# Kernel optimization log

Hardware: AMD Instinct MI355X
Metric: run time of the kernel (lower is better)

The kernel has to match this reference:

```python
import jax, jax.numpy as jnp
import numpy as np

TEAM = 5
N_PLAYER = 131072
PD = 256
HD = 256
MLP_H = 512
B = 16384

def _combine(t=TEAM):
    i1, i2 = [], []
    for i in range(t):
        for j in range(t):
            if i != j:
                i1.append(i); i2.append(j)
    return np.array(i1), np.array(i2)

IDX1, IDX2 = _combine()

def setup_inputs() -> dict:
    key = jax.random.key(0)
    ks = jax.random.split(key, 12)
    def xavier(k, shape):
        fan_in, fan_out = shape[1], shape[0]
        std = np.sqrt(2.0 / (fan_in + fan_out))
        return (jax.random.normal(k, shape, dtype=jnp.float32) * std)
    return {
        'team_ids': jax.random.randint(ks[0], (B, TEAM), 0, N_PLAYER),
        'emb': xavier(ks[1], (N_PLAYER, PD)),
        'fm_w1': xavier(ks[2], (2 * HD, PD)),
        'fm_b1': jnp.zeros((2 * HD,), jnp.float32),
        'fm_w2': xavier(ks[3], (HD, 2 * HD)),
        'fm_b2': jnp.zeros((HD,), jnp.float32),
        'att_w': xavier(ks[4], (HD, HD)),
        'att_b': jnp.zeros((HD,), jnp.float32),
        'mlp_w1': xavier(ks[5], (MLP_H, HD)),
        'mlp_b1': jnp.zeros((MLP_H,), jnp.float32),
        'mlp_w2': xavier(ks[6], (1, MLP_H)),
        'mlp_b2': jnp.zeros((1,), jnp.float32),
    }

def reference(team_ids, emb, fm_w1, fm_b1, fm_w2, fm_b2, att_w, att_b,
              mlp_w1, mlp_b1, mlp_w2, mlp_b2):
    # embedding lookup: [B, 5, PD]
    x = emb[team_ids]
    # feature mapper: Linear -> SiLU -> Linear  => [B, 5, HD]
    h = jax.nn.silu(jnp.einsum('btp,hp->bth', x, fm_w1) + fm_b1)
    h = jnp.einsum('bth,oh->bto', h, fm_w2) + fm_b2
    # pairwise gather (20 ordered pairs): [B, 20, HD]
    a = h[:, IDX1]
    b = h[:, IDX2]
    prod = a * b
    # small MLP (dropout is inference identity): [B, 20]
    m = jax.nn.silu(jnp.einsum('bph,mh->bpm', prod, mlp_w1) + mlp_b1)
    order2 = (jnp.einsum('bpm,om->bpo', m, mlp_w2) + mlp_b2)[..., 0]
    # attention (reduce=True -> view [B, 5, 4, HD], softmax over axis 2)
    wa = jnp.einsum('bph,oh->bpo', a, att_w) + att_b
    score = (wa * b).sum(-1).reshape(-1, TEAM, TEAM - 1)
    normal = jax.nn.softmax(score, axis=2).reshape(-1, TEAM * (TEAM - 1))
    order2 = order2 * normal
    return order2.sum(axis=1, keepdims=True)  # [B, 1]
```

## Files before the change

kernel.cpp:

```cpp
#include <hip/hip_runtime.h>

#define NB     16384
#define TEAM   5
#define NPAIR  20
#define UPAIR  10
#define PD     256
#define HD     256
#define H1D    512
#define NPLAY  (NB*TEAM)
#define NCHUNK 1

typedef __attribute__((ext_vector_type(4))) float f32x4;
typedef __attribute__((ext_vector_type(8))) short s16x8;

__device__ __forceinline__ float silu_f(float x){ return x / (1.0f + __expf(-x)); }

__device__ __forceinline__ unsigned short bf16_rne(float x){
  unsigned u = __float_as_uint(x);
  unsigned r = u + 0x7fffu + ((u >> 16) & 1u);
  return (unsigned short)(r >> 16);
}
__device__ __forceinline__ float bf16_to_f(unsigned short s){
  return __uint_as_float(((unsigned)s) << 16);
}
__device__ __forceinline__ void tsplit(float x, short& h, short& l){
  const unsigned u = __float_as_uint(x);
  h = (short)(u >> 16);
  const float lf = x - __uint_as_float(u & 0xffff0000u);
  l = (short)(__float_as_uint(lf) >> 16);
}

__global__ void k_pack(const float* __restrict__ w, short* __restrict__ wf,
                       int KT, int total)
{
  const int tid = blockIdx.x * 256 + threadIdx.x;
  if (tid >= total) return;
  const int slot = tid & 7;
  const int lane = (tid >> 3) & 63;
  const int grp  = tid >> 9;
  const int kt   = grp % KT;
  const int nt   = grp / KT;
  const int K    = KT * 32;
  const int n = nt * 16 + (lane & 15);
  const int k = kt * 32 + ((lane >> 4) << 3) + slot;
  const float v = w[(size_t)n * K + k];
  const unsigned short hi = bf16_rne(v);
  const float lo = v - bf16_to_f(hi);
  wf[tid]         = (short)hi;
  wf[total + tid] = (short)bf16_rne(lo);
}

__global__ __launch_bounds__(256) void k_l1(
    const int* __restrict__ tids, const float* __restrict__ emb,
    const short* __restrict__ w1f, const float* __restrict__ b1,
    float* __restrict__ Hh1)
{
  __shared__ short Af[10240];
  __shared__ float Bb[256];
  __shared__ int   Tid[80];

  const int t = threadIdx.x, lane = t & 63, w = t >> 6;
  const int bx = blockIdx.x, cy = blockIdx.y;
  const int p0 = bx * 80;

  if (t < 80) Tid[t] = tids[p0 + t];
  Bb[t] = b1[cy * 256 + t];

  f32x4 acc[5][4];
  #pragma unroll
  for (int mt = 0; mt < 5; ++mt)
    #pragma unroll
    for (int j = 0; j < 4; ++j) acc[mt][j] = (f32x4){0.f,0.f,0.f,0.f};

  const s16x8* Bh = reinterpret_cast<const s16x8*>(w1f);

  for (int kt = 0; kt < 8; ++kt) {
    const int kc = kt >> 1, ks = kt & 1;
    if (ks == 0) {
      __syncthreads();
      const int kt0 = kc * 64;
      #pragma unroll
      for (int f = 0; f < 5; ++f) {
        const int idx4  = t + f * 256;
        const int sg    = (idx4 & 1) * 4;
        const int lane_ = (idx4 >> 1) & 63;
        const int ks_   = (idx4 >> 7) & 1;
        const int mt_   = idx4 >> 8;
        const int p     = mt_ * 16 + (lane_ & 15);
        const int k     = kt0 + ks_ * 32 + ((lane_ >> 4) << 3) + sg;
        const int row   = Tid[p];
        const float4 a4 = *reinterpret_cast<const float4*>(emb + (size_t)row * PD + k);
        float pv[4] = {a4.x, a4.y, a4.z, a4.w};
        short hi[4], lo[4];
        #pragma unroll
        for (int e = 0; e < 4; ++e) tsplit(pv[e], hi[e], lo[e]);
        const int aoff = (mt_ * 2 + ks_) * 512 + lane_ * 8 + sg;
        *reinterpret_cast<short4*>(&Af[aoff])        = make_short4(hi[0],hi[1],hi[2],hi[3]);
        *reinterpret_cast<short4*>(&Af[5120 + aoff]) = make_short4(lo[0],lo[1],lo[2],lo[3]);
      }
      __syncthreads();
    }

    s16x8 ah[5], al[5];
    #pragma unroll
    for (int mt = 0; mt < 5; ++mt) {
      ah[mt] = *reinterpret_cast<const s16x8*>(&Af[(mt*2 + ks)*512 + lane*8]);
      al[mt] = *reinterpret_cast<const s16x8*>(&Af[5120 + (mt*2 + ks)*512 + lane*8]);
    }
    #pragma unroll
    for (int j = 0; j < 4; ++j) {
      const int nt = cy * 16 + w * 4 + j;
      const s16x8 bh = Bh[(nt*8 + kt)*64 + lane];
      const s16x8 bl = Bh[16384 + (nt*8 + kt)*64 + lane];
      #pragma unroll
      for (int mt = 0; mt < 5; ++mt) {
        acc[mt][j] = __builtin_amdgcn_mfma_f32_16x16x32_bf16(ah[mt], bh, acc[mt][j], 0,0,0);
        acc[mt][j] = __builtin_amdgcn_mfma_f32_16x16x32_bf16(al[mt], bh, acc[mt][j], 0,0,0);
        acc[mt][j] = __builtin_amdgcn_mfma_f32_16x16x32_bf16(ah[mt], bl, acc[mt][j], 0,0,0);
      }
    }
  }

  #pragma unroll
  for (int mt = 0; mt < 5; ++mt)
    #pragma unroll
    for (int j = 0; j < 4; ++j) {
      const int nl = w * 64 + j * 16 + (lane & 15);
      const int n  = cy * 256 + nl;
      #pragma unroll
      for (int r = 0; r < 4; ++r) {
        const int p = p0 + mt*16 + ((lane >> 4) << 2) + r;
        Hh1[(size_t)p * H1D + n] = silu_f(acc[mt][j][r] + Bb[nl]);
      }
    }
}

__global__ __launch_bounds__(256) void k_l2(
    const float* __restrict__ Hh1, const short* __restrict__ w2f,
    const float* __restrict__ b2, float* __restrict__ Hout)
{
  __shared__ short Af[10240];
  __shared__ float Bb[256];

  const int t = threadIdx.x, lane = t & 63, w = t >> 6;
  const int bx = blockIdx.x;
  const int p0 = bx * 80;

  Bb[t] = b2[t];

  const int sg    = (t & 1) * 4;
  const int lane_ = (t >> 1) & 63;
  const int ks_   = (t >> 7) & 1;
  const int kb    = ks_ * 32 + ((lane_ >> 4) << 3) + sg;
  int rowH[5], aof[5];
  #pragma unroll
  for (int f = 0; f < 5; ++f) {
    rowH[f] = (p0 + f * 16 + (lane_ & 15)) * H1D;
    aof[f]  = (f * 2 + ks_) * 512 + lane_ * 8 + sg;
  }

  f32x4 acc[5][4];
  #pragma unroll
  for (int mt = 0; mt < 5; ++mt)
    #pragma unroll
    for (int j = 0; j < 4; ++j) acc[mt][j] = (f32x4){0.f,0.f,0.f,0.f};

  const s16x8* B2 = reinterpret_cast<const s16x8*>(w2f);

  for (int kt = 0; kt < 16; ++kt) {
    const int kc = kt >> 1, ks = kt & 1;
    if (ks == 0) {
      __syncthreads();
      const int kk = kc * 64 + kb;
      #pragma unroll
      for (int f = 0; f < 5; ++f) {
        const float4 a4 = *reinterpret_cast<const float4*>(Hh1 + rowH[f] + kk);
        float pv[4] = {a4.x, a4.y, a4.z, a4.w};
        short hi[4], lo[4];
        #pragma unroll
        for (int e = 0; e < 4; ++e) tsplit(pv[e], hi[e], lo[e]);
        *reinterpret_cast<short4*>(&Af[aof[f]])        = make_short4(hi[0],hi[1],hi[2],hi[3]);
        *reinterpret_cast<short4*>(&Af[5120 + aof[f]]) = make_short4(lo[0],lo[1],lo[2],lo[3]);
      }
      __syncthreads();
    }

    s16x8 ah[5], al[5];
    #pragma unroll
    for (int mt = 0; mt < 5; ++mt) {
      ah[mt] = *reinterpret_cast<const s16x8*>(&Af[(mt*2 + ks)*512 + lane*8]);
      al[mt] = *reinterpret_cast<const s16x8*>(&Af[5120 + (mt*2 + ks)*512 + lane*8]);
    }
    #pragma unroll
    for (int j = 0; j < 4; ++j) {
      const int nt = w * 4 + j;
      const s16x8 bh = B2[(nt*16 + kt)*64 + lane];
      const s16x8 bl = B2[16384 + (nt*16 + kt)*64 + lane];
      #pragma unroll
      for (int mt = 0; mt < 5; ++mt) {
        acc[mt][j] = __builtin_amdgcn_mfma_f32_16x16x32_bf16(ah[mt], bh, acc[mt][j], 0,0,0);
        acc[mt][j] = __builtin_amdgcn_mfma_f32_16x16x32_bf16(al[mt], bh, acc[mt][j], 0,0,0);
        acc[mt][j] = __builtin_amdgcn_mfma_f32_16x16x32_bf16(ah[mt], bl, acc[mt][j], 0,0,0);
      }
    }
  }

  #pragma unroll
  for (int mt = 0; mt < 5; ++mt)
    #pragma unroll
    for (int j = 0; j < 4; ++j) {
      const int n = w * 64 + j * 16 + (lane & 15);
      #pragma unroll
      for (int r = 0; r < 4; ++r) {
        const int p = p0 + mt*16 + ((lane >> 4) << 2) + r;
        Hout[(size_t)p * PD + n] = acc[mt][j][r] + Bb[n];
      }
    }
}

__global__ __launch_bounds__(256) void k_fm4(
    const int* __restrict__ tids, const float* __restrict__ emb,
    const short* __restrict__ w1f, const float* __restrict__ b1,
    const short* __restrict__ w2f, const float* __restrict__ b2,
    float* __restrict__ Hout)
{
  __shared__ char smem[65536 + 3072];
  short* Af  = reinterpret_cast<short*>(smem);
  short* H1f = reinterpret_cast<short*>(smem);
  float* Bb  = reinterpret_cast<float*>(smem + 65536);

  const int t = threadIdx.x, lane = t & 63, w = t >> 6;
  const int m0 = blockIdx.x * 32;

  Bb[t]       = b1[t];
  Bb[t + 256] = b1[t + 256];
  Bb[t + 512] = b2[t];

  #pragma unroll
  for (int f = 0; f < 8; ++f) {
    const int g     = t + f * 256;
    const int sg    = (g & 1) * 4;
    const int lane_ = (g >> 1) & 63;
    const int kt_   = (g >> 7) & 7;
    const int mt_   = g >> 10;
    const int p     = mt_ * 16 + (lane_ & 15);
    const int k     = kt_ * 32 + ((lane_ >> 4) << 3) + sg;
    const int row   = tids[m0 + p];
    const float4 a4 = *reinterpret_cast<const float4*>(emb + (size_t)row * PD + k);
    float pv[4] = {a4.x, a4.y, a4.z, a4.w};
    short hi[4], lo[4];
    #pragma unroll
    for (int e = 0; e < 4; ++e) {
      const unsigned short h = bf16_rne(pv[e]);
      hi[e] = (short)h;
      lo[e] = (short)bf16_rne(pv[e] - bf16_to_f(h));
    }
    const int off = ((mt_*8 + kt_)*64 + lane_)*8 + sg;
    *reinterpret_cast<short4*>(&Af[off])        = make_short4(hi[0],hi[1],hi[2],hi[3]);
    *reinterpret_cast<short4*>(&Af[8192 + off]) = make_short4(lo[0],lo[1],lo[2],lo[3]);
  }
  __syncthreads();

  const s16x8* B1 = reinterpret_cast<const s16x8*>(w1f);
  const s16x8* B2 = reinterpret_cast<const s16x8*>(w2f);

  f32x4 acc1[2][8];
  #pragma unroll
  for (int mt = 0; mt < 2; ++mt)
    #pragma unroll
    for (int j = 0; j < 8; ++j) acc1[mt][j] = (f32x4){0.f,0.f,0.f,0.f};

  #pragma unroll
  for (int kt = 0; kt < 8; ++kt) {
    s16x8 ah[2], al[2];
    #pragma unroll
    for (int mt = 0; mt < 2; ++mt) {
      ah[mt] = *reinterpret_cast<const s16x8*>(&Af[((mt*8 + kt)*64 + lane)*8]);
      al[mt] = *reinterpret_cast<const s16x8*>(&Af[8192 + ((mt*8 + kt)*64 + lane)*8]);
    }
    #pragma unroll
    for (int j = 0; j < 8; ++j) {
      const int nt = w * 8 + j;
      const s16x8 bh = B1[(nt*8 + kt)*64 + lane];
      const s16x8 bl = B1[16384 + (nt*8 + kt)*64 + lane];
      #pragma unroll
      for (int mt = 0; mt < 2; ++mt) {
        acc1[mt][j] = __builtin_amdgcn_mfma_f32_16x16x32_bf16(ah[mt], bh, acc1[mt][j], 0,0,0);
        acc1[mt][j] = __builtin_amdgcn_mfma_f32_16x16x32_bf16(al[mt], bh, acc1[mt][j], 0,0,0);
        acc1[mt][j] = __builtin_amdgcn_mfma_f32_16x16x32_bf16(ah[mt], bl, acc1[mt][j], 0,0,0);
      }
    }
  }
  __syncthreads();

  #pragma unroll
  for (int mt = 0; mt < 2; ++mt)
    #pragma unroll
    for (int j = 0; j < 8; ++j) {
      const int n     = w * 128 + j * 16 + (lane & 15);
      const int kt2   = n >> 5;
      const int lhalf = 16 * ((n >> 3) & 3);
      const int slot2 = n & 7;
      #pragma unroll
      for (int r = 0; r < 4; ++r) {
        const int prow = ((lane >> 4) << 2) + r;
        const float v = silu_f(acc1[mt][j][r] + Bb[n]);
        const unsigned short hi = bf16_rne(v);
        const int off = ((mt*16 + kt2)*64 + lhalf + prow)*8 + slot2;
        H1f[off]         = (short)hi;
        H1f[16384 + off] = (short)bf16_rne(v - bf16_to_f(hi));
      }
    }
  __syncthreads();

  f32x4 acc2[2][4];
  #pragma unroll
  for (int mt = 0; mt < 2; ++mt)
    #pragma unroll
    for (int j = 0; j < 4; ++j) acc2[mt][j] = (f32x4){0.f,0.f,0.f,0.f};

  #pragma unroll
  for (int kt = 0; kt < 16; ++kt) {
    s16x8 ah[2], al[2];
    #pragma unroll
    for (int mt = 0; mt < 2; ++mt) {
      ah[mt] = *reinterpret_cast<const s16x8*>(&H1f[((mt*16 + kt)*64 + lane)*8]);
      al[mt] = *reinterpret_cast<const s16x8*>(&H1f[16384 + ((mt*16 + kt)*64 + lane)*8]);
    }
    #pragma unroll
    for (int j = 0; j < 4; ++j) {
      const int nt = w * 4 + j;
      const s16x8 bh = B2[(nt*16 + kt)*64 + lane];
      const s16x8 bl = B2[16384 + (nt*16 + kt)*64 + lane];
      #pragma unroll
      for (int mt = 0; mt < 2; ++mt) {
        acc2[mt][j] = __builtin_amdgcn_mfma_f32_16x16x32_bf16(ah[mt], bh, acc2[mt][j], 0,0,0);
        acc2[mt][j] = __builtin_amdgcn_mfma_f32_16x16x32_bf16(al[mt], bh, acc2[mt][j], 0,0,0);
        acc2[mt][j] = __builtin_amdgcn_mfma_f32_16x16x32_bf16(ah[mt], bl, acc2[mt][j], 0,0,0);
      }
    }
  }

  #pragma unroll
  for (int mt = 0; mt < 2; ++mt)
    #pragma unroll
    for (int j = 0; j < 4; ++j) {
      const int n = w * 64 + j * 16 + (lane & 15);
      #pragma unroll
      for (int r = 0; r < 4; ++r) {
        const int p = m0 + mt*16 + ((lane >> 4) << 2) + r;
        Hout[(size_t)p * PD + n] = acc2[mt][j][r] + Bb[512 + n];
      }
    }
}

__global__ __launch_bounds__(256) void k_score(
    const float* __restrict__ Hin, const short* __restrict__ attf,
    const float* __restrict__ attb, float* __restrict__ SC)
{
  __shared__ char smem[49152 + 1024];
  short* Hf  = reinterpret_cast<short*>(smem);
  float* WAl = reinterpret_cast<float*>(smem);
  float* Ab  = reinterpret_cast<float*>(smem + 49152);

  const int t = threadIdx.x, lane = t & 63, w = t >> 6;
  const int b0 = blockIdx.x * 8;
  const float* src = Hin + (size_t)b0 * TEAM * PD;

  Ab[t] = attb[t];

  #pragma unroll
  for (int f = 0; f < 12; ++f) {
    const int g     = t + f * 256;
    const int sg    = (g & 1) * 4;
    const int lane_ = (g >> 1) & 63;
    const int kt_   = (g >> 7) & 7;
    const int mt_   = g >> 10;
    const int p     = mt_ * 16 + (lane_ & 15);
    const int k     = kt_ * 32 + ((lane_ >> 4) << 3) + sg;
    float4 a4 = make_float4(0.f, 0.f, 0.f, 0.f);
    if (p < 40) a4 = *reinterpret_cast<const float4*>(src + (size_t)p * PD + k);
    float pv[4] = {a4.x, a4.y, a4.z, a4.w};
    short hi[4], lo[4];
    #pragma unroll
    for (int e = 0; e < 4; ++e) tsplit(pv[e], hi[e], lo[e]);
    const int off = ((mt_*8 + kt_)*64 + lane_)*8 + sg;
    *reinterpret_cast<short4*>(&Hf[off])         = make_short4(hi[0],hi[1],hi[2],hi[3]);
    *reinterpret_cast<short4*>(&Hf[12288 + off]) = make_short4(lo[0],lo[1],lo[2],lo[3]);
  }
  __syncthreads();

  f32x4 acc[3][4];
  #pragma unroll
  for (int mt = 0; mt < 3; ++mt)
    #pragma unroll
    for (int j = 0; j < 4; ++j) acc[mt][j] = (f32x4){0.f,0.f,0.f,0.f};

  const s16x8* Bh = reinterpret_cast<const s16x8*>(attf);
  #pragma unroll
  for (int kt = 0; kt < 8; ++kt) {
    s16x8 ah[3], al[3];
    #pragma unroll
    for (int mt = 0; mt < 3; ++mt) {
      ah[mt] = *reinterpret_cast<const s16x8*>(&Hf[((mt*8 + kt)*64 + lane)*8]);
      al[mt] = *reinterpret_cast<const s16x8*>(&Hf[12288 + ((mt*8 + kt)*64 + lane)*8]);
    }
    #pragma unroll
    for (int j = 0; j < 4; ++j) {
      const int nt = w * 4 + j;
      const s16x8 bh = Bh[(nt*8 + kt)*64 + lane];
      const s16x8 bl = Bh[8192 + (nt*8 + kt)*64 + lane];
      #pragma unroll
      for (int mt = 0; mt < 3; ++mt) {
        acc[mt][j] = __builtin_amdgcn_mfma_f32_16x16x32_bf16(ah[mt], bh, acc[mt][j], 0,0,0);
        acc[mt][j] = __builtin_amdgcn_mfma_f32_16x16x32_bf16(al[mt], bh, acc[mt][j], 0,0,0);
        acc[mt][j] = __builtin_amdgcn_mfma_f32_16x16x32_bf16(ah[mt], bl, acc[mt][j], 0,0,0);
      }
    }
  }
  __syncthreads();

  #pragma unroll
  for (int mt = 0; mt < 3; ++mt)
    #pragma unroll
    for (int j = 0; j < 4; ++j) {
      const int n = w * 64 + j * 16 + (lane & 15);
      #pragma unroll
      for (int r = 0; r < 4; ++r) {
        const int row = mt * 16 + ((lane >> 4) << 2) + r;
        if (row < 40) WAl[row * 260 + n] = acc[mt][j][r] + Ab[n];
      }
    }
  __syncthreads();

  #pragma unroll
  for (int qq = 0; qq < 2; ++qq) {
    const int q = w * 2 + qq;
    #pragma unroll
    for (int p = 0; p < NPAIR; ++p) {
      const int i1 = p >> 2, jj = p & 3;
      const int i2 = jj + (jj >= i1 ? 1 : 0);
      const float4 a4 = *reinterpret_cast<const float4*>(WAl + (q*TEAM + i1) * 260 + lane * 4);
      const float4 b4 = *reinterpret_cast<const float4*>(src + (size_t)(q*TEAM + i2) * PD + lane * 4);
      float v = a4.x*b4.x + a4.y*b4.y + a4.z*b4.z + a4.w*b4.w;
      #pragma unroll
      for (int off = 32; off > 0; off >>= 1) v += __shfl_xor(v, off);
      if (lane == 0) SC[(size_t)(b0 + q) * NPAIR + p] = v;
    }
  }
}

__global__ __launch_bounds__(256, 2) void k_mlp(
    const float* __restrict__ Hin, const short* __restrict__ w1f,
    const float* __restrict__ b1, const float* __restrict__ w2,
    float* __restrict__ PART)
{
  __shared__ float Hl[40*260];
  __shared__ short Af[10240];
  __shared__ float Wb[512];
  __shared__ float Ww[512];

  const int t    = threadIdx.x;
  const int lane = t & 63;
  const int w    = t >> 6;
  const int blkx = blockIdx.x;
  const int b0   = blkx * 8;
  const float* src = Hin + (size_t)b0 * TEAM * PD;

  {
    #pragma unroll
    for (int rep = 0; rep < 10; ++rep) {
      const int flat = t + rep * 256;
      const int row = flat >> 6, c4 = (flat & 63) * 4;
      *reinterpret_cast<float4*>(Hl + row * 260 + c4) =
        *reinterpret_cast<const float4*>(src + (size_t)row * PD + c4);
    }
    Wb[t]       = b1[t];
    Wb[t + 256] = b1[t + 256];
    Ww[t]       = w2[t];
    Ww[t + 256] = w2[t + 256];
  }

  const int sg    = (t & 1) * 4;
  const int lane_ = (t >> 1) & 63;
  const int ks_   = (t >> 7) & 1;
  const int kb    = ks_ * 32 + ((lane_ >> 4) << 3) + sg;
  int rowA[5], rowB[5], aof[5];
  #pragma unroll
  for (int f = 0; f < 5; ++f) {
    const int r  = f * 16 + (lane_ & 15);
    const int q  = r / UPAIR;
    const int p  = r - q * UPAIR;
    const int i1 = (p >= 4) + (p >= 7) + (p >= 9);
    const int i2 = p - (i1 * (9 - i1)) / 2 + i1 + 1;
    rowA[f] = (q * TEAM + i1) * 260;
    rowB[f] = (q * TEAM + i2) * 260;
    aof[f]  = (f * 2 + ks_) * 512 + lane_ * 8 + sg;
  }

  f32x4 acc[5][8];
  #pragma unroll
  for (int mt = 0; mt < 5; ++mt)
    #pragma unroll
    for (int j = 0; j < 8; ++j) acc[mt][j] = (f32x4){0.f,0.f,0.f,0.f};

  const s16x8* Bh = reinterpret_cast<const s16x8*>(w1f);
  const s16x8* Bl = reinterpret_cast<const s16x8*>(w1f + 131072);
  const int nt0 = w * 8;

  for (int kt = 0; kt < 8; ++kt) {
    const int kc = kt >> 1, ks = kt & 1;
    if (ks == 0) {
      __syncthreads();
      const int kk = kc * 64 + kb;
      #pragma unroll
      for (int f = 0; f < 5; ++f) {
        const float4 a4 = *reinterpret_cast<const float4*>(Hl + rowA[f] + kk);
        const float4 b4 = *reinterpret_cast<const float4*>(Hl + rowB[f] + kk);
        float pv[4] = {a4.x*b4.x, a4.y*b4.y, a4.z*b4.z, a4.w*b4.w};
        short hi[4], lo[4];
        #pragma unroll
        for (int e = 0; e < 4; ++e) tsplit(pv[e], hi[e], lo[e]);
        *reinterpret_cast<short4*>(&Af[aof[f]])        = make_short4(hi[0],hi[1],hi[2],hi[3]);
        *reinterpret_cast<short4*>(&Af[5120 + aof[f]]) = make_short4(lo[0],lo[1],lo[2],lo[3]);
      }
      __syncthreads();
    }

    s16x8 ah[5], al[5];
    #pragma unroll
    for (int mt = 0; mt < 5; ++mt) {
      ah[mt] = *reinterpret_cast<const s16x8*>(&Af[(mt*2 + ks)*512 + lane*8]);
      al[mt] = *reinterpret_cast<const s16x8*>(&Af[5120 + (mt*2 + ks)*512 + lane*8]);
    }
    #pragma unroll
    for (int j = 0; j < 8; ++j) {
      const s16x8 bh = Bh[((nt0 + j)*8 + kt)*64 + lane];
      const s16x8 bl = Bl[((nt0 + j)*8 + kt)*64 + lane];
      #pragma unroll
      for (int mt = 0; mt < 5; ++mt) {
        acc[mt][j] = __builtin_amdgcn_mfma_f32_16x16x32_bf16(ah[mt], bh, acc[mt][j], 0,0,0);
        acc[mt][j] = __builtin_amdgcn_mfma_f32_16x16x32_bf16(ah[mt], bl, acc[mt][j], 0,0,0);
        acc[mt][j] = __builtin_amdgcn_mfma_f32_16x16x32_bf16(al[mt], bh, acc[mt][j], 0,0,0);
      }
    }
  }

  __syncthreads();
  float* red = reinterpret_cast<float*>(Af);

  const int colbase = w * 128 + (lane & 15);
  #pragma unroll
  for (int mt = 0; mt < 5; ++mt)
    #pragma unroll
    for (int r = 0; r < 4; ++r) {
      float s = 0.0f;
      #pragma unroll
      for (int j = 0; j < 8; ++j) {
        const int c = colbase + j * 16;
        s += silu_f(acc[mt][j][r] + Wb[c]) * Ww[c];
      }
      s += __shfl_xor(s, 1); s += __shfl_xor(s, 2);
      s += __shfl_xor(s, 4); s += __shfl_xor(s, 8);
      if ((lane & 15) == 0) {
        const int row = mt * 16 + ((lane >> 4) << 2) + r;
        red[row * 4 + w] = s;
      }
    }
  __syncthreads();
  if (t < 80) {
    const float s = red[t*4] + red[t*4+1] + red[t*4+2] + red[t*4+3];
    PART[(size_t)blkx * 80 + t] = s;
  }
}

__global__ void k_final(const float* __restrict__ SC, const float* __restrict__ PART,
                        const float* __restrict__ mb2, float* __restrict__ out)
{
  const int b = blockIdx.x * 256 + threadIdx.x;
  if (b >= NB) return;
  const float bias2 = mb2[0];
  float ord[UPAIR];
  #pragma unroll
  for (int u = 0; u < UPAIR; ++u) {
    float s = bias2;
    #pragma unroll
    for (int g = 0; g < NCHUNK; ++g) s += PART[(size_t)g * (NB*UPAIR) + (size_t)b * UPAIR + u];
    ord[u] = s;
  }
  float sc[NPAIR];
  #pragma unroll
  for (int p = 0; p < NPAIR; ++p) sc[p] = SC[(size_t)b * NPAIR + p];

  float res = 0.0f;
  #pragma unroll
  for (int i = 0; i < TEAM; ++i) {
    float m = sc[4*i];
    #pragma unroll
    for (int jj = 1; jj < 4; ++jj) m = fmaxf(m, sc[4*i + jj]);
    float e[4], d = 0.0f;
    #pragma unroll
    for (int jj = 0; jj < 4; ++jj) { e[jj] = __expf(sc[4*i + jj] - m); d += e[jj]; }
    const float inv = 1.0f / d;
    #pragma unroll
    for (int jj = 0; jj < 4; ++jj) {
      const int i2 = jj + (jj >= i ? 1 : 0);
      const int a  = i < i2 ? i : i2;
      const int bb = i < i2 ? i2 : i;
      const int u  = (a * (9 - a)) / 2 + (bb - a - 1);
      res += ord[u] * e[jj] * inv;
    }
  }
  out[b] = res;
}

extern "C" void kernel_launch(void* const* d_in, const int* in_sizes, int n_in,
                              void* d_out, int out_size, void* d_ws, size_t ws_size,
                              hipStream_t stream)
{
  (void)in_sizes; (void)n_in; (void)out_size;
  const int*   tids = (const int*)  d_in[0];
  const float* emb  = (const float*)d_in[1];
  const float* fw1  = (const float*)d_in[2];
  const float* fb1  = (const float*)d_in[3];
  const float* fw2  = (const float*)d_in[4];
  const float* fb2  = (const float*)d_in[5];
  const float* attw = (const float*)d_in[6];
  const float* attb = (const float*)d_in[7];
  const float* mw1  = (const float*)d_in[8];
  const float* mb1  = (const float*)d_in[9];
  const float* mw2  = (const float*)d_in[10];
  const float* mb2  = (const float*)d_in[11];
  float* out = (float*)d_out;

  float* H     = (float*)d_ws;
  float* SC    = H + (size_t)NPLAY * PD;
  float* PART  = SC + (size_t)NB * NPAIR;
  short* w1f_m = (short*)(PART + (size_t)NCHUNK * NB * UPAIR);
  short* w1f_f = w1f_m + 262144;
  short* w2f_f = w1f_f + 262144;
  short* attf  = w2f_f + 262144;
  float* Hh1   = (float*)(attf + 131072);
  const size_t NEED = (size_t)((char*)(Hh1 + (size_t)NPLAY * H1D) - (char*)d_ws);

  k_pack<<<512, 256, 0, stream>>>(mw1, w1f_m, 8, 131072);
  k_pack<<<512, 256, 0, stream>>>(fw1, w1f_f, 8, 131072);
  k_pack<<<512, 256, 0, stream>>>(fw2, w2f_f, 16, 131072);
  k_pack<<<256, 256, 0, stream>>>(attw, attf, 8, 65536);

  if (ws_size >= NEED) {
    k_l1<<<dim3(NPLAY/80, 2), 256, 0, stream>>>(tids, emb, w1f_f, fb1, Hh1);
    k_l2<<<NPLAY/80, 256, 0, stream>>>(Hh1, w2f_f, fb2, H);
  } else {
    k_fm4<<<NPLAY/32, 256, 0, stream>>>(tids, emb, w1f_f, fb1, w2f_f, fb2, H);
  }
  k_score<<<NB/8, 256, 0, stream>>>(H, attf, attb, SC);
  k_mlp<<<NB/8, 256, 0, stream>>>(H, w1f_m, mb1, mw2, PART);
  k_final<<<NB/256, 256, 0, stream>>>(SC, PART, mb2, out);
}
```

Measured before the change: 602.0 us.

## Double-buffer LDS A tiles and prefetch next chunk in feature-mapper GEMMs

In the two feature-mapper GEMM kernels (k_l1, k_l2), the single shared A tile becomes a two-slot ring buffer. The next K-chunk of embedding or hidden rows is loaded into registers before the MFMA work on the current chunk, which cuts one barrier per chunk and lets global-load latency overlap with compute. The price is twice the LDS for A and extra registers for the prefetched float4s, which may lower occupancy.

```diff
diff --git a/kernel.cpp b/kernel.cpp
--- a/kernel.cpp
+++ b/kernel.cpp
@@ -55,7 +55,7 @@
     const short* __restrict__ w1f, const float* __restrict__ b1,
     float* __restrict__ Hh1)
 {
-  __shared__ short Af[10240];
+  __shared__ short Af[2][10240];
   __shared__ float Bb[256];
   __shared__ int   Tid[80];
 
@@ -65,6 +65,18 @@
 
   if (t < 80) Tid[t] = tids[p0 + t];
   Bb[t] = b1[cy * 256 + t];
+  __syncthreads();
+
+  const int sg    = (t & 1) * 4;
+  const int lane_ = (t >> 1) & 63;
+  const int ks_   = (t >> 7) & 1;
+  const int kb    = ks_ * 32 + ((lane_ >> 4) << 3) + sg;
+  int rowE[5], aof[5];
+  #pragma unroll
+  for (int f = 0; f < 5; ++f) {
+    rowE[f] = Tid[f * 16 + (lane_ & 15)] * PD;
+    aof[f]  = (f * 2 + ks_) * 512 + lane_ * 8 + sg;
+  }
 
   f32x4 acc[5][4];
   #pragma unroll
@@ -74,49 +86,50 @@
 
   const s16x8* Bh = reinterpret_cast<const s16x8*>(w1f);
 
-  for (int kt = 0; kt < 8; ++kt) {
-    const int kc = kt >> 1, ks = kt & 1;
-    if (ks == 0) {
-      __syncthreads();
-      const int kt0 = kc * 64;
-      #pragma unroll
-      for (int f = 0; f < 5; ++f) {
-        const int idx4  = t + f * 256;
-        const int sg    = (idx4 & 1) * 4;
-        const int lane_ = (idx4 >> 1) & 63;
-        const int ks_   = (idx4 >> 7) & 1;
-        const int mt_   = idx4 >> 8;
-        const int p     = mt_ * 16 + (lane_ & 15);
-        const int k     = kt0 + ks_ * 32 + ((lane_ >> 4) << 3) + sg;
-        const int row   = Tid[p];
-        const float4 a4 = *reinterpret_cast<const float4*>(emb + (size_t)row * PD + k);
-        float pv[4] = {a4.x, a4.y, a4.z, a4.w};
-        short hi[4], lo[4];
+  float4 ld[5];
+  #pragma unroll
+  for (int f = 0; f < 5; ++f)
+    ld[f] = *reinterpret_cast<const float4*>(emb + rowE[f] + kb);
+
+  for (int kc = 0; kc < 4; ++kc) {
+    short* buf = Af[kc & 1];
+    #pragma unroll
+    for (int f = 0; f < 5; ++f) {
+      float pv[4] = {ld[f].x, ld[f].y, ld[f].z, ld[f].w};
+      short hi[4], lo[4];
+      #pragma unroll
+      for (int e = 0; e < 4; ++e) tsplit(pv[e], hi[e], lo[e]);
+      *reinterpret_cast<short4*>(&buf[aof[f]])        = make_short4(hi[0],hi[1],hi[2],hi[3]);
+      *reinterpret_cast<short4*>(&buf[5120 + aof[f]]) = make_short4(lo[0],lo[1],lo[2],lo[3]);
+    }
+    if (kc < 3) {
+      const int kk = (kc + 1) * 64 + kb;
+      #pragma unroll
+      for (int f = 0; f < 5; ++f)
+        ld[f] = *reinterpret_cast<const float4*>(emb + rowE[f] + kk);
+    }
+    __syncthreads();
+
+    #pragma unroll
+    for (int ks = 0; ks < 2; ++ks) {
+      const int kt = kc * 2 + ks;
+      s16x8 ah[5], al[5];
+      #pragma unroll
+      for (int mt = 0; mt < 5; ++mt) {
+        ah[mt] = *reinterpret_cast<const s16x8*>(&buf[(mt*2 + ks)*512 + lane*8]);
+        al[mt] = *reinterpret_cast<const s16x8*>(&buf[5120 + (mt*2 + ks)*512 + lane*8]);
+      }
+      #pragma unroll
+      for (int j = 0; j < 4; ++j) {
+        const int nt = cy * 16 + w * 4 + j;
+        const s16x8 bh = Bh[(nt*8 + kt)*64 + lane];
+        const s16x8 bl = Bh[16384 + (nt*8 + kt)*64 + lane];
         #pragma unroll
-        for (int e = 0; e < 4; ++e) tsplit(pv[e], hi[e], lo[e]);
-        const int aoff = (mt_ * 2 + ks_) * 512 + lane_ * 8 + sg;
-        *reinterpret_cast<short4*>(&Af[aoff])        = make_short4(hi[0],hi[1],hi[2],hi[3]);
-        *reinterpret_cast<short4*>(&Af[5120 + aoff]) = make_short4(lo[0],lo[1],lo[2],lo[3]);
-      }
-      __syncthreads();
-    }
-
-    s16x8 ah[5], al[5];
-    #pragma unroll
-    for (int mt = 0; mt < 5; ++mt) {
-      ah[mt] = *reinterpret_cast<const s16x8*>(&Af[(mt*2 + ks)*512 + lane*8]);
-      al[mt] = *reinterpret_cast<const s16x8*>(&Af[5120 + (mt*2 + ks)*512 + lane*8]);
-    }
-    #pragma unroll
-    for (int j = 0; j < 4; ++j) {
-      const int nt = cy * 16 + w * 4 + j;
-      const s16x8 bh = Bh[(nt*8 + kt)*64 + lane];
-      const s16x8 bl = Bh[16384 + (nt*8 + kt)*64 + lane];
-      #pragma unroll
-      for (int mt = 0; mt < 5; ++mt) {
-        acc[mt][j] = __builtin_amdgcn_mfma_f32_16x16x32_bf16(ah[mt], bh, acc[mt][j], 0,0,0);
-        acc[mt][j] = __builtin_amdgcn_mfma_f32_16x16x32_bf16(al[mt], bh, acc[mt][j], 0,0,0);
-        acc[mt][j] = __builtin_amdgcn_mfma_f32_16x16x32_bf16(ah[mt], bl, acc[mt][j], 0,0,0);
+        for (int mt = 0; mt < 5; ++mt) {
+          acc[mt][j] = __builtin_amdgcn_mfma_f32_16x16x32_bf16(ah[mt], bh, acc[mt][j], 0,0,0);
+          acc[mt][j] = __builtin_amdgcn_mfma_f32_16x16x32_bf16(al[mt], bh, acc[mt][j], 0,0,0);
+          acc[mt][j] = __builtin_amdgcn_mfma_f32_16x16x32_bf16(ah[mt], bl, acc[mt][j], 0,0,0);
+        }
       }
     }
   }
@@ -139,7 +152,7 @@
     const float* __restrict__ Hh1, const short* __restrict__ w2f,
     const float* __restrict__ b2, float* __restrict__ Hout)
 {
-  __shared__ short Af[10240];
+  __shared__ short Af[2][10240];
   __shared__ float Bb[256];
 
   const int t = threadIdx.x, lane = t & 63, w = t >> 6;
@@ -167,40 +180,50 @@
 
   const s16x8* B2 = reinterpret_cast<const s16x8*>(w2f);
 
-  for (int kt = 0; kt < 16; ++kt) {
-    const int kc = kt >> 1, ks = kt & 1;
-    if (ks == 0) {
-      __syncthreads();
-      const int kk = kc * 64 + kb;
-      #pragma unroll
-      for (int f = 0; f < 5; ++f) {
-        const float4 a4 = *reinterpret_cast<const float4*>(Hh1 + rowH[f] + kk);
-        float pv[4] = {a4.x, a4.y, a4.z, a4.w};
-        short hi[4], lo[4];
+  float4 ld[5];
+  #pragma unroll
+  for (int f = 0; f < 5; ++f)
+    ld[f] = *reinterpret_cast<const float4*>(Hh1 + rowH[f] + kb);
+
+  for (int kc = 0; kc < 8; ++kc) {
+    short* buf = Af[kc & 1];
+    #pragma unroll
+    for (int f = 0; f < 5; ++f) {
+      float pv[4] = {ld[f].x, ld[f].y, ld[f].z, ld[f].w};
+      short hi[4], lo[4];
+      #pragma unroll
+      for (int e = 0; e < 4; ++e) tsplit(pv[e], hi[e], lo[e]);
+      *reinterpret_cast<short4*>(&buf[aof[f]])        = make_short4(hi[0],hi[1],hi[2],hi[3]);
+      *reinterpret_cast<short4*>(&buf[5120 + aof[f]]) = make_short4(lo[0],lo[1],lo[2],lo[3]);
+    }
+    if (kc < 7) {
+      const int kk = (kc + 1) * 64 + kb;
+      #pragma unroll
+      for (int f = 0; f < 5; ++f)
+        ld[f] = *reinterpret_cast<const float4*>(Hh1 + rowH[f] + kk);
+    }
+    __syncthreads();
+
+    #pragma unroll
+    for (int ks = 0; ks < 2; ++ks) {
+      const int kt = kc * 2 + ks;
+      s16x8 ah[5], al[5];
+      #pragma unroll
+      for (int mt = 0; mt < 5; ++mt) {
+        ah[mt] = *reinterpret_cast<const s16x8*>(&buf[(mt*2 + ks)*512 + lane*8]);
+        al[mt] = *reinterpret_cast<const s16x8*>(&buf[5120 + (mt*2 + ks)*512 + lane*8]);
+      }
+      #pragma unroll
+      for (int j = 0; j < 4; ++j) {
+        const int nt = w * 4 + j;
+        const s16x8 bh = B2[(nt*16 + kt)*64 + lane];
+        const s16x8 bl = B2[16384 + (nt*16 + kt)*64 + lane];
         #pragma unroll
-        for (int e = 0; e < 4; ++e) tsplit(pv[e], hi[e], lo[e]);
-        *reinterpret_cast<short4*>(&Af[aof[f]])        = make_short4(hi[0],hi[1],hi[2],hi[3]);
-        *reinterpret_cast<short4*>(&Af[5120 + aof[f]]) = make_short4(lo[0],lo[1],lo[2],lo[3]);
-      }
-      __syncthreads();
-    }
-
-    s16x8 ah[5], al[5];
-    #pragma unroll
-    for (int mt = 0; mt < 5; ++mt) {
-      ah[mt] = *reinterpret_cast<const s16x8*>(&Af[(mt*2 + ks)*512 + lane*8]);
-      al[mt] = *reinterpret_cast<const s16x8*>(&Af[5120 + (mt*2 + ks)*512 + lane*8]);
-    }
-    #pragma unroll
-    for (int j = 0; j < 4; ++j) {
-      const int nt = w * 4 + j;
-      const s16x8 bh = B2[(nt*16 + kt)*64 + lane];
-      const s16x8 bl = B2[16384 + (nt*16 + kt)*64 + lane];
-      #pragma unroll
-      for (int mt = 0; mt < 5; ++mt) {
-        acc[mt][j] = __builtin_amdgcn_mfma_f32_16x16x32_bf16(ah[mt], bh, acc[mt][j], 0,0,0);
-        acc[mt][j] = __builtin_amdgcn_mfma_f32_16x16x32_bf16(al[mt], bh, acc[mt][j], 0,0,0);
-        acc[mt][j] = __builtin_amdgcn_mfma_f32_16x16x32_bf16(ah[mt], bl, acc[mt][j], 0,0,0);
+        for (int mt = 0; mt < 5; ++mt) {
+          acc[mt][j] = __builtin_amdgcn_mfma_f32_16x16x32_bf16(ah[mt], bh, acc[mt][j], 0,0,0);
+          acc[mt][j] = __builtin_amdgcn_mfma_f32_16x16x32_bf16(al[mt], bh, acc[mt][j], 0,0,0);
+          acc[mt][j] = __builtin_amdgcn_mfma_f32_16x16x32_bf16(ah[mt], bl, acc[mt][j], 0,0,0);
+        }
       }
     }
   }
```

After: 647.6 us. 7.6% more time.

## Split MLP hidden dimension across two grid chunks and read H directly from global

Applied to the files above, without the earlier changes.

The MLP kernel now launches a second grid dimension so that each block computes half of the 512 hidden units. Partial sums go to separate PART slices, which the final kernel adds up. The LDS staging of H is removed, and pair products are read straight from global memory instead. This halves the accumulator registers and LDS per block, which should allow more blocks per CU. The cost is that each H tile is loaded twice (once per chunk), and global reads may be uncoalesced or repeated within a block.

```diff
diff --git a/kernel.cpp b/kernel.cpp
--- a/kernel.cpp
+++ b/kernel.cpp
@@ -8,7 +8,7 @@
 #define HD     256
 #define H1D    512
 #define NPLAY  (NB*TEAM)
-#define NCHUNK 1
+#define NCHUNK 2
 
 typedef __attribute__((ext_vector_type(4))) float f32x4;
 typedef __attribute__((ext_vector_type(8))) short s16x8;
@@ -450,36 +450,26 @@
   }
 }
 
-__global__ __launch_bounds__(256, 2) void k_mlp(
+__global__ __launch_bounds__(256) void k_mlp(
     const float* __restrict__ Hin, const short* __restrict__ w1f,
     const float* __restrict__ b1, const float* __restrict__ w2,
     float* __restrict__ PART)
 {
-  __shared__ float Hl[40*260];
   __shared__ short Af[10240];
-  __shared__ float Wb[512];
-  __shared__ float Ww[512];
+  __shared__ float Wb[256];
+  __shared__ float Ww[256];
+  __shared__ float red[320];
 
   const int t    = threadIdx.x;
   const int lane = t & 63;
   const int w    = t >> 6;
   const int blkx = blockIdx.x;
+  const int cy   = blockIdx.y;
   const int b0   = blkx * 8;
   const float* src = Hin + (size_t)b0 * TEAM * PD;
 
-  {
-    #pragma unroll
-    for (int rep = 0; rep < 10; ++rep) {
-      const int flat = t + rep * 256;
-      const int row = flat >> 6, c4 = (flat & 63) * 4;
-      *reinterpret_cast<float4*>(Hl + row * 260 + c4) =
-        *reinterpret_cast<const float4*>(src + (size_t)row * PD + c4);
-    }
-    Wb[t]       = b1[t];
-    Wb[t + 256] = b1[t + 256];
-    Ww[t]       = w2[t];
-    Ww[t + 256] = w2[t + 256];
-  }
+  Wb[t & 255] = b1[cy * 256 + (t & 255)];
+  Ww[t & 255] = w2[cy * 256 + (t & 255)];
 
   const int sg    = (t & 1) * 4;
   const int lane_ = (t >> 1) & 63;
@@ -493,20 +483,20 @@
     const int p  = r - q * UPAIR;
     const int i1 = (p >= 4) + (p >= 7) + (p >= 9);
     const int i2 = p - (i1 * (9 - i1)) / 2 + i1 + 1;
-    rowA[f] = (q * TEAM + i1) * 260;
-    rowB[f] = (q * TEAM + i2) * 260;
+    rowA[f] = (q * TEAM + i1) * PD;
+    rowB[f] = (q * TEAM + i2) * PD;
     aof[f]  = (f * 2 + ks_) * 512 + lane_ * 8 + sg;
   }
 
-  f32x4 acc[5][8];
+  f32x4 acc[5][4];
   #pragma unroll
   for (int mt = 0; mt < 5; ++mt)
     #pragma unroll
-    for (int j = 0; j < 8; ++j) acc[mt][j] = (f32x4){0.f,0.f,0.f,0.f};
+    for (int j = 0; j < 4; ++j) acc[mt][j] = (f32x4){0.f,0.f,0.f,0.f};
 
   const s16x8* Bh = reinterpret_cast<const s16x8*>(w1f);
   const s16x8* Bl = reinterpret_cast<const s16x8*>(w1f + 131072);
-  const int nt0 = w * 8;
+  const int nt0 = cy * 16 + w * 4;
 
   for (int kt = 0; kt < 8; ++kt) {
     const int kc = kt >> 1, ks = kt & 1;
@@ -515,8 +505,8 @@
       const int kk = kc * 64 + kb;
       #pragma unroll
       for (int f = 0; f < 5; ++f) {
-        const float4 a4 = *reinterpret_cast<const float4*>(Hl + rowA[f] + kk);
-        const float4 b4 = *reinterpret_cast<const float4*>(Hl + rowB[f] + kk);
+        const float4 a4 = *reinterpret_cast<const float4*>(src + rowA[f] + kk);
+        const float4 b4 = *reinterpret_cast<const float4*>(src + rowB[f] + kk);
         float pv[4] = {a4.x*b4.x, a4.y*b4.y, a4.z*b4.z, a4.w*b4.w};
         short hi[4], lo[4];
         #pragma unroll
@@ -534,7 +524,7 @@
       al[mt] = *reinterpret_cast<const s16x8*>(&Af[5120 + (mt*2 + ks)*512 + lane*8]);
     }
     #pragma unroll
-    for (int j = 0; j < 8; ++j) {
+    for (int j = 0; j < 4; ++j) {
       const s16x8 bh = Bh[((nt0 + j)*8 + kt)*64 + lane];
       const s16x8 bl = Bl[((nt0 + j)*8 + kt)*64 + lane];
       #pragma unroll
@@ -547,16 +537,15 @@
   }
 
   __syncthreads();
-  float* red = reinterpret_cast<float*>(Af);
-
-  const int colbase = w * 128 + (lane & 15);
+
+  const int colbase = w * 64 + (lane & 15);
   #pragma unroll
   for (int mt = 0; mt < 5; ++mt)
     #pragma unroll
     for (int r = 0; r < 4; ++r) {
       float s = 0.0f;
       #pragma unroll
-      for (int j = 0; j < 8; ++j) {
+      for (int j = 0; j < 4; ++j) {
         const int c = colbase + j * 16;
         s += silu_f(acc[mt][j][r] + Wb[c]) * Ww[c];
       }
@@ -570,7 +559,7 @@
   __syncthreads();
   if (t < 80) {
     const float s = red[t*4] + red[t*4+1] + red[t*4+2] + red[t*4+3];
-    PART[(size_t)blkx * 80 + t] = s;
+    PART[(size_t)cy * (NB*UPAIR) + (size_t)blkx * 80 + t] = s;
   }
 }
 
@@ -655,6 +644,6 @@
     k_fm4<<<NPLAY/32, 256, 0, stream>>>(tids, emb, w1f_f, fb1, w2f_f, fb2, H);
   }
   k_score<<<NB/8, 256, 0, stream>>>(H, attf, attb, SC);
-  k_mlp<<<NB/8, 256, 0, stream>>>(H, w1f_m, mb1, mw2, PART);
+  k_mlp<<<dim3(NB/8, 2), 256, 0, stream>>>(H, w1f_m, mb1, mw2, PART);
   k_final<<<NB/256, 256, 0, stream>>>(SC, PART, mb2, out);
 }
```

New measurement: 598.7 us. No clear change (-0.6%).
